# Kernel optimization log

Hardware: AMD Instinct MI355X
Metric: run time of the kernel (lower is better)

## Reference

```python
import jax, jax.numpy as jnp
import numpy as np

N = 131072        # total nodes (256 graphs x 512 nodes)
E = 2097152       # edges (avg degree 16)
F_IN = 64
HID = 64
T = 8             # timesteps
NUM_GRAPHS = 256
NPG = 512         # nodes per graph (uniform -> n >= T branch of _node_blur)
H_CLF = 64
CLASSES = 10
NUM_STEPS = 4
BETA = 0.9
THR = 1.0
SLOPE = 25.0      # snntorch surrogate.fast_sigmoid default slope

@jax.custom_vjp
def spike_fn(v):
    # heaviside forward, fast-sigmoid surrogate backward (snn.Leaky spike)
    return (v > 0).astype(v.dtype)

def _spk_fwd(v):
    return spike_fn(v), v

def _spk_bwd(v, g):
    return (g / (SLOPE * jnp.abs(v) + 1.0) ** 2,)

spike_fn.defvjp(_spk_fwd, _spk_bwd)

def gcn_conv(x, src, dst, w, b):
    # PyG GCNConv: add self loops, symmetric normalization, aggregate src->dst
    h = x @ w
    loop = jnp.arange(N, dtype=src.dtype)
    s = jnp.concatenate([src, loop])
    d = jnp.concatenate([dst, loop])
    deg = jax.ops.segment_sum(jnp.ones(s.shape, h.dtype), d, num_segments=N)
    dinv = jnp.where(deg > 0, jax.lax.rsqrt(jnp.maximum(deg, 1e-12)), 0.0)
    msg = h[s] * (dinv[s] * dinv[d])[:, None]          # [E+N, HID]
    return jax.ops.segment_sum(msg, d, num_segments=N) + b

def lif_rate(x):
    # snn.Leaky (reset_mechanism='subtract'): reset from previous mem (detached),
    # mem = beta*mem + x - reset*thr, spk = heaviside(mem - thr); mean spike rate.
    def step(mem, _):
        reset = jax.lax.stop_gradient((mem > THR).astype(x.dtype))
        mem = BETA * mem + x - reset * THR
        return mem, spike_fn(mem - THR)
    _, spks = jax.lax.scan(step, jnp.zeros_like(x), None, length=NUM_STEPS)
    return spks.mean(axis=0)

def node_blur(x):
    # uniform graphs, n = NPG >= T: reshape each graph to (r, T, F) and
    # combine chunks with weights linspace(thr, 0, r)
    r = NPG // T
    w = jnp.linspace(THR, 0.0, r, dtype=x.dtype)
    xg = x.reshape(NUM_GRAPHS, r, T, HID)
    return jnp.einsum('r,grtf->gtf', w, xg)             # [G, T, HID]

def setup_inputs() -> dict:
    key = jax.random.key(0)
    ks = jax.random.split(key, 8)
    x = jax.random.normal(ks[0], (N, F_IN), jnp.float32)
    edge_index = jax.random.randint(ks[1], (2, E), 0, N, jnp.int32)
    batch = (jnp.arange(N) // NPG).astype(jnp.int32)
    def lin(k, fi, fo):
        s = 1.0 / np.sqrt(fi)
        k1, k2 = jax.random.split(k)
        return (jax.random.uniform(k1, (fi, fo), jnp.float32, -s, s),
                jax.random.uniform(k2, (fo,), jnp.float32, -s, s))
    conv1_w, conv1_b = lin(ks[2], F_IN, HID)
    conv2_w, conv2_b = lin(ks[3], HID, HID)
    lin1_w, lin1_b = lin(ks[4], HID * T, H_CLF)
    lin2_w, lin2_b = lin(ks[5], H_CLF, H_CLF)
    lin3_w, lin3_b = lin(ks[6], H_CLF, CLASSES)
    return dict(x=x, edge_index=edge_index, batch=batch,
                conv1_w=conv1_w, conv1_b=conv1_b, conv2_w=conv2_w, conv2_b=conv2_b,
                lin1_w=lin1_w, lin1_b=lin1_b, lin2_w=lin2_w, lin2_b=lin2_b,
                lin3_w=lin3_w, lin3_b=lin3_b)

def reference(x, edge_index, batch, conv1_w, conv1_b, conv2_w, conv2_b,
              lin1_w, lin1_b, lin2_w, lin2_b, lin3_w, lin3_b):
    src, dst = edge_index[0], edge_index[1]
    h = gcn_conv(x, src, dst, conv1_w, conv1_b)
    h = jax.nn.relu(h)                                   # dropout: eval-mode identity
    h = gcn_conv(h, src, dst, conv2_w, conv2_b)
    z = node_blur(h)                                     # [G, T, HID]
    z = z.reshape(NUM_GRAPHS, T * HID)
    z = lif_rate(z @ lin1_w + lin1_b)
    z = lif_rate(z @ lin2_w + lin2_b)
    return z @ lin3_w + lin3_b                           # [G, CLASSES]
```

## Files before the change

kernel.cpp:

```cpp
#include <hip/hip_runtime.h>
#include <hip/hip_bf16.h>

#define NN 131072
#define EE 2097152
#define NG 256
#define TT 8
#define NB 512
#define NBLK 1024
#define SCAP 16
#define MAXW 32
#define OVFA_CAP 4096
#define OVFB_CAP 16384

__global__ __launch_bounds__(256) void k_zero_i(int* __restrict__ p, int n) {
  int i = blockIdx.x * 256 + threadIdx.x;
  if (i < n) p[i] = 0;
}

__global__ __launch_bounds__(256) void k_part2(const int* __restrict__ ei, int* __restrict__ pairs,
                                               int* __restrict__ cnt2, int* __restrict__ ovfAcnt,
                                               int2* __restrict__ ovfA) {
  __shared__ int lcur[NB];
  int tid = threadIdx.x, blk = blockIdx.x;
  lcur[tid] = 0; lcur[tid + 256] = 0;
  __syncthreads();
  int e0 = blk * (EE / NBLK);
#pragma unroll
  for (int i = 0; i < (EE / NBLK) / 256; ++i) {
    int e = e0 + i * 256 + tid;
    int s = ei[e], d = ei[EE + e];
    int b = d >> 8;
    int k = atomicAdd(&lcur[b], 1);
    if (k < SCAP)
      pairs[((size_t)blk * NB + b) * SCAP + k] = ((d & 255) << 17) | s;
    else {
      int oi = atomicAdd(ovfAcnt, 1);
      if (oi < OVFA_CAP) ovfA[oi] = make_int2(d, s);
    }
  }
  __syncthreads();
  cnt2[(size_t)blk * NB + tid] = min(lcur[tid], SCAP);
  cnt2[(size_t)blk * NB + tid + 256] = min(lcur[tid + 256], SCAP);
}

__global__ __launch_bounds__(256) void k_bucket(const int* __restrict__ pairs, const int* __restrict__ cnt2,
                                                int* __restrict__ col, int* __restrict__ cnt,
                                                const int* __restrict__ ovfAcnt, const int2* __restrict__ ovfA,
                                                int* __restrict__ ovfBcnt, int2* __restrict__ ovfB) {
  __shared__ int lcnt[256];
  __shared__ int lell[256 * MAXW];
  __shared__ int scnt[NBLK];
  int b = blockIdx.x, tid = threadIdx.x;
  lcnt[tid] = 0;
#pragma unroll
  for (int i = 0; i < NBLK / 256; ++i)
    scnt[tid + i * 256] = cnt2[(size_t)(tid + i * 256) * NB + b];
  __syncthreads();
  for (int idx = tid; idx < NBLK * SCAP; idx += 256) {
    int blk = idx >> 4, slot = idx & (SCAP - 1);
    if (slot < scnt[blk]) {
      int p = pairs[(size_t)blk * (NB * SCAP) + b * SCAP + slot];
      int s = p & 0x1FFFF, dl = p >> 17;
      int k = atomicAdd(&lcnt[dl], 1);
      if (k < MAXW) lell[dl * MAXW + k] = s;
      else {
        int oi = atomicAdd(ovfBcnt, 1);
        if (oi < OVFB_CAP) ovfB[oi] = make_int2(b * 256 + dl, s);
      }
    }
  }
  int na = min(*ovfAcnt, OVFA_CAP);
  for (int i = tid; i < na; i += 256) {
    int d = ovfA[i].x, s = ovfA[i].y;
    if ((d >> 8) == b) {
      int dl = d & 255;
      int k = atomicAdd(&lcnt[dl], 1);
      if (k < MAXW) lell[dl * MAXW + k] = s;
      else {
        int oi = atomicAdd(ovfBcnt, 1);
        if (oi < OVFB_CAP) ovfB[oi] = make_int2(d, s);
      }
    }
  }
  __syncthreads();
  int4* dst4 = (int4*)(col + (size_t)b * 256 * MAXW);
  const int4* src4 = (const int4*)lell;
#pragma unroll
  for (int i = 0; i < (256 * MAXW / 4) / 256; ++i)
    dst4[tid + i * 256] = src4[tid + i * 256];
  cnt[b * 256 + tid] = lcnt[tid];
}

__global__ __launch_bounds__(256) void k_gemm(const float* __restrict__ X, const float* __restrict__ W,
                                              const float* __restrict__ bias_in, int relu_bias,
                                              float* __restrict__ Y) {
  __shared__ float xs[64 * 64];
  __shared__ float ws[64 * 64];
  int tid = threadIdx.x;
  size_t row0 = (size_t)blockIdx.x * 64;
#pragma unroll
  for (int i = 0; i < 16; ++i) ws[tid + i * 256] = W[tid + i * 256];
#pragma unroll
  for (int i = 0; i < 4; ++i) {
    int idx = tid + i * 256;
    int r = idx >> 4, q = idx & 15;
    float4 v = ((const float4*)(X + (row0 + r) * 64))[q];
    if (relu_bias) {
      int c0 = q * 4;
      v.x = fmaxf(v.x + bias_in[c0 + 0], 0.f);
      v.y = fmaxf(v.y + bias_in[c0 + 1], 0.f);
      v.z = fmaxf(v.z + bias_in[c0 + 2], 0.f);
      v.w = fmaxf(v.w + bias_in[c0 + 3], 0.f);
    }
    *(float4*)&xs[idx * 4] = v;
  }
  __syncthreads();
  int c = tid & 63, rg = tid >> 6;
  float acc[16];
#pragma unroll
  for (int i = 0; i < 16; ++i) acc[i] = 0.f;
#pragma unroll 4
  for (int kq = 0; kq < 16; ++kq) {
    float w0 = ws[(kq * 4 + 0) * 64 + c];
    float w1 = ws[(kq * 4 + 1) * 64 + c];
    float w2 = ws[(kq * 4 + 2) * 64 + c];
    float w3 = ws[(kq * 4 + 3) * 64 + c];
#pragma unroll
    for (int i = 0; i < 16; ++i) {
      const float4 xv = *(const float4*)&xs[(rg + i * 4) * 64 + kq * 4];
      acc[i] += xv.x * w0 + xv.y * w1 + xv.z * w2 + xv.w * w3;
    }
  }
#pragma unroll
  for (int i = 0; i < 16; ++i)
    Y[(row0 + rg + (size_t)i * 4) * 64 + c] = acc[i];
}

__global__ __launch_bounds__(256) void k_gather_ell(const float* __restrict__ H, const int* __restrict__ cnt,
                                                    const int* __restrict__ col, float* __restrict__ agg) {
  int lane = threadIdx.x & 63;
  int n0 = (blockIdx.x * 4 + (threadIdx.x >> 6)) * 2;
  int n1 = n0 + 1;
  int deg0 = cnt[n0], deg1 = cnt[n1];
  float dn0 = rsqrtf((float)deg0 + 1.0f), dn1 = rsqrtf((float)deg1 + 1.0f);
  float acc0 = H[(size_t)n0 * 64 + lane] * (dn0 * dn0);
  float acc1 = H[(size_t)n1 * 64 + lane] * (dn1 * dn1);
  int m0 = min(deg0, MAXW), m1 = min(deg1, MAXW);
  const int* c0r = col + (size_t)n0 * MAXW;
  const int* c1r = col + (size_t)n1 * MAXW;
  int myc0 = (lane < m0) ? c0r[lane] : 0;
  int myc1 = (lane < m1) ? c1r[lane] : 0;
  float md0 = (lane < m0) ? rsqrtf((float)cnt[myc0] + 1.0f) : 0.f;
  float md1 = (lane < m1) ? rsqrtf((float)cnt[myc1] + 1.0f) : 0.f;
  int mm = max(m0, m1);
  for (int j = 0; j < mm; j += 4) {
    float h[8], cc[8];
#pragma unroll
    for (int k = 0; k < 4; ++k) {
      if (j + k < m0) {
        int s = __shfl(myc0, j + k);
        cc[k] = __shfl(md0, j + k);
        h[k] = H[(size_t)s * 64 + lane];
      } else { h[k] = 0.f; cc[k] = 0.f; }
      if (j + k < m1) {
        int s = __shfl(myc1, j + k);
        cc[4 + k] = __shfl(md1, j + k);
        h[4 + k] = H[(size_t)s * 64 + lane];
      } else { h[4 + k] = 0.f; cc[4 + k] = 0.f; }
    }
#pragma unroll
    for (int k = 0; k < 4; ++k) {
      acc0 += h[k] * (cc[k] * dn0);
      acc1 += h[4 + k] * (cc[4 + k] * dn1);
    }
  }
  agg[(size_t)n0 * 64 + lane] = acc0;
  agg[(size_t)n1 * 64 + lane] = acc1;
}

__global__ __launch_bounds__(64) void k_ovf(const int2* __restrict__ ovf, const int* __restrict__ ovfcnt,
                                            const int* __restrict__ cnt, const float* __restrict__ H,
                                            float* __restrict__ agg) {
  int lane = threadIdx.x;
  int n = min(*ovfcnt, OVFB_CAP);
  for (int i = blockIdx.x; i < n; i += gridDim.x) {
    int d = ovf[i].x, s = ovf[i].y;
    float v = H[(size_t)s * 64 + lane] * rsqrtf((float)cnt[s] + 1.0f) * rsqrtf((float)cnt[d] + 1.0f);
    atomicAdd(&agg[(size_t)d * 64 + lane], v);
  }
}

__global__ __launch_bounds__(256) void k_blur(const float* __restrict__ agg2, const float* __restrict__ b2,
                                              float* __restrict__ z) {
  int idx = blockIdx.x * 256 + threadIdx.x;
  if (idx >= NG * TT * 64) return;
  int f = idx & 63, t = (idx >> 6) & 7, g = idx >> 9;
  const float* base = agg2 + ((size_t)g * 512 + (size_t)t) * 64 + f;
  float acc = 0.f;
#pragma unroll
  for (int rr = 0; rr < 64; ++rr) {
    float w = (float)(63 - rr) * (1.0f / 63.0f);
    acc += w * base[(size_t)rr * 8 * 64];
  }
  z[idx] = acc + 32.0f * b2[f];
}

__global__ __launch_bounds__(64) void k_head(const float* __restrict__ z,
    const float* __restrict__ w1, const float* __restrict__ b1,
    const float* __restrict__ w2, const float* __restrict__ b2,
    const float* __restrict__ w3, const float* __restrict__ b3,
    float* __restrict__ out) {
  __shared__ float zs[512];
  __shared__ float r[64];
  int g = blockIdx.x, c = threadIdx.x;
#pragma unroll
  for (int i = 0; i < 8; ++i) zs[c + i * 64] = z[(size_t)g * 512 + c + i * 64];
  __syncthreads();
  float a = b1[c];
  for (int j = 0; j < 512; ++j) a += zs[j] * w1[j * 64 + c];
  float mem = 0.f, rate = 0.f;
#pragma unroll
  for (int s = 0; s < 4; ++s) {
    float reset = (mem > 1.0f) ? 1.0f : 0.0f;
    mem = 0.9f * mem + a - reset;
    if (mem - 1.0f > 0.0f) rate += 1.0f;
  }
  r[c] = rate * 0.25f;
  __syncthreads();
  float a2 = b2[c];
#pragma unroll
  for (int j = 0; j < 64; ++j) a2 += r[j] * w2[j * 64 + c];
  __syncthreads();
  mem = 0.f; rate = 0.f;
#pragma unroll
  for (int s = 0; s < 4; ++s) {
    float reset = (mem > 1.0f) ? 1.0f : 0.0f;
    mem = 0.9f * mem + a2 - reset;
    if (mem - 1.0f > 0.0f) rate += 1.0f;
  }
  r[c] = rate * 0.25f;
  __syncthreads();
  if (c < 10) {
    float o = b3[c];
#pragma unroll
    for (int j = 0; j < 64; ++j) o += r[j] * w3[j * 10 + c];
    out[(size_t)g * 10 + c] = o;
  }
}

extern "C" void kernel_launch(void* const* d_in, const int* in_sizes, int n_in,
                              void* d_out, int out_size, void* d_ws, size_t ws_size,
                              hipStream_t stream) {
  const float* x   = (const float*)d_in[0];
  const int*   ei  = (const int*)d_in[1];
  const float* c1w = (const float*)d_in[3];
  const float* c1b = (const float*)d_in[4];
  const float* c2w = (const float*)d_in[5];
  const float* c2b = (const float*)d_in[6];
  const float* l1w = (const float*)d_in[7];
  const float* l1b = (const float*)d_in[8];
  const float* l2w = (const float*)d_in[9];
  const float* l2b = (const float*)d_in[10];
  const float* l3w = (const float*)d_in[11];
  const float* l3b = (const float*)d_in[12];
  float* out = (float*)d_out;

  char* w = (char*)d_ws;
  size_t off = 0;
  float* bufA = (float*)(w + off); off += (size_t)NN * 64 * 4;
  float* bufB = (float*)(w + off); off += (size_t)NN * 64 * 4;
  int* col    = (int*)(w + off);   off += (size_t)NN * MAXW * 4;
  int* cnt    = (int*)(w + off);   off += (size_t)NN * 4;
  int* cnt2   = (int*)(w + off);   off += (size_t)NBLK * NB * 4;
  float* z    = (float*)(w + off); off += (size_t)NG * TT * 64 * 4;
  int* meta   = (int*)(w + off);   off += 16 * 4;
  int2* ovfA  = (int2*)(w + off);  off += (size_t)OVFA_CAP * 8;
  int2* ovfB  = (int2*)(w + off);  off += (size_t)OVFB_CAP * 8;
  int* ovfAcnt = meta;
  int* ovfBcnt = meta + 1;
  int* pairs   = (int*)bufA;

  k_zero_i<<<1, 256, 0, stream>>>(meta, 16);
  k_part2<<<NBLK, 256, 0, stream>>>(ei, pairs, cnt2, ovfAcnt, ovfA);
  k_bucket<<<NB, 256, 0, stream>>>(pairs, cnt2, col, cnt, ovfAcnt, ovfA, ovfBcnt, ovfB);

  k_gemm<<<NN / 64, 256, 0, stream>>>(x, c1w, nullptr, 0, bufA);
  k_gather_ell<<<NN / 8, 256, 0, stream>>>(bufA, cnt, col, bufB);
  k_ovf<<<32, 64, 0, stream>>>(ovfB, ovfBcnt, cnt, bufA, bufB);

  k_gemm<<<NN / 64, 256, 0, stream>>>(bufB, c2w, c1b, 1, bufA);
  k_gather_ell<<<NN / 8, 256, 0, stream>>>(bufA, cnt, col, bufB);
  k_ovf<<<32, 64, 0, stream>>>(ovfB, ovfBcnt, cnt, bufA, bufB);

  k_blur<<<NG * TT * 64 / 256, 256, 0, stream>>>(bufB, c2b, z);
  k_head<<<NG, 64, 0, stream>>>(z, l1w, l1b, l2w, l2b, l3w, l3b, out);
}
```

Measured before the change: 327.6 us.

## Move conv2 weight matmul past aggregation and blur, fuse overflow into gather

Because aggregation and the blur are linear, the conv2 weight multiply now runs after the node blur on the small per-graph tensor inside the head kernel, which removes the second full-size GEMM. Bias and ReLU are applied on the fly while the second gather loads each neighbour. The overflow edges are handled inside the gather kernel by a linear scan, replacing the separate atomic kernel. Per-block bucket counts are also stored as bytes instead of ints. The risk is that every warp scans the whole overflow list, which costs a lot if that list is large, and some floating-point results change slightly because of the reordering.

```diff
diff --git a/kernel.cpp b/kernel.cpp
--- a/kernel.cpp
+++ b/kernel.cpp
@@ -18,7 +18,7 @@
 }
 
 __global__ __launch_bounds__(256) void k_part2(const int* __restrict__ ei, int* __restrict__ pairs,
-                                               int* __restrict__ cnt2, int* __restrict__ ovfAcnt,
+                                               unsigned char* __restrict__ cnt2, int* __restrict__ ovfAcnt,
                                                int2* __restrict__ ovfA) {
   __shared__ int lcur[NB];
   int tid = threadIdx.x, blk = blockIdx.x;
@@ -39,17 +39,17 @@
     }
   }
   __syncthreads();
-  cnt2[(size_t)blk * NB + tid] = min(lcur[tid], SCAP);
-  cnt2[(size_t)blk * NB + tid + 256] = min(lcur[tid + 256], SCAP);
-}
-
-__global__ __launch_bounds__(256) void k_bucket(const int* __restrict__ pairs, const int* __restrict__ cnt2,
+  cnt2[(size_t)blk * NB + tid] = (unsigned char)min(lcur[tid], SCAP);
+  cnt2[(size_t)blk * NB + tid + 256] = (unsigned char)min(lcur[tid + 256], SCAP);
+}
+
+__global__ __launch_bounds__(256) void k_bucket(const int* __restrict__ pairs, const unsigned char* __restrict__ cnt2,
                                                 int* __restrict__ col, int* __restrict__ cnt,
                                                 const int* __restrict__ ovfAcnt, const int2* __restrict__ ovfA,
                                                 int* __restrict__ ovfBcnt, int2* __restrict__ ovfB) {
   __shared__ int lcnt[256];
   __shared__ int lell[256 * MAXW];
-  __shared__ int scnt[NBLK];
+  __shared__ unsigned char scnt[NBLK];
   int b = blockIdx.x, tid = threadIdx.x;
   lcnt[tid] = 0;
 #pragma unroll
@@ -58,7 +58,7 @@
   __syncthreads();
   for (int idx = tid; idx < NBLK * SCAP; idx += 256) {
     int blk = idx >> 4, slot = idx & (SCAP - 1);
-    if (slot < scnt[blk]) {
+    if (slot < (int)scnt[blk]) {
       int p = pairs[(size_t)blk * (NB * SCAP) + b * SCAP + slot];
       int s = p & 0x1FFFF, dl = p >> 17;
       int k = atomicAdd(&lcnt[dl], 1);
@@ -92,7 +92,6 @@
 }
 
 __global__ __launch_bounds__(256) void k_gemm(const float* __restrict__ X, const float* __restrict__ W,
-                                              const float* __restrict__ bias_in, int relu_bias,
                                               float* __restrict__ Y) {
   __shared__ float xs[64 * 64];
   __shared__ float ws[64 * 64];
@@ -105,13 +104,6 @@
     int idx = tid + i * 256;
     int r = idx >> 4, q = idx & 15;
     float4 v = ((const float4*)(X + (row0 + r) * 64))[q];
-    if (relu_bias) {
-      int c0 = q * 4;
-      v.x = fmaxf(v.x + bias_in[c0 + 0], 0.f);
-      v.y = fmaxf(v.y + bias_in[c0 + 1], 0.f);
-      v.z = fmaxf(v.z + bias_in[c0 + 2], 0.f);
-      v.w = fmaxf(v.w + bias_in[c0 + 3], 0.f);
-    }
     *(float4*)&xs[idx * 4] = v;
   }
   __syncthreads();
@@ -136,15 +128,23 @@
     Y[(row0 + rg + (size_t)i * 4) * 64 + c] = acc[i];
 }
 
-__global__ __launch_bounds__(256) void k_gather_ell(const float* __restrict__ H, const int* __restrict__ cnt,
-                                                    const int* __restrict__ col, float* __restrict__ agg) {
+template <int RELU>
+__global__ __launch_bounds__(256) void k_gather(const float* __restrict__ H, const int* __restrict__ cnt,
+                                                const int* __restrict__ col,
+                                                const int* __restrict__ ovfcnt, const int2* __restrict__ ovf,
+                                                const float* __restrict__ bias, float* __restrict__ agg) {
   int lane = threadIdx.x & 63;
   int n0 = (blockIdx.x * 4 + (threadIdx.x >> 6)) * 2;
   int n1 = n0 + 1;
+  float b = RELU ? bias[lane] : 0.f;
+  auto ld = [&](int s) -> float {
+    float v = H[(size_t)s * 64 + lane];
+    return RELU ? fmaxf(v + b, 0.f) : v;
+  };
   int deg0 = cnt[n0], deg1 = cnt[n1];
   float dn0 = rsqrtf((float)deg0 + 1.0f), dn1 = rsqrtf((float)deg1 + 1.0f);
-  float acc0 = H[(size_t)n0 * 64 + lane] * (dn0 * dn0);
-  float acc1 = H[(size_t)n1 * 64 + lane] * (dn1 * dn1);
+  float acc0 = ld(n0) * (dn0 * dn0);
+  float acc1 = ld(n1) * (dn1 * dn1);
   int m0 = min(deg0, MAXW), m1 = min(deg1, MAXW);
   const int* c0r = col + (size_t)n0 * MAXW;
   const int* c1r = col + (size_t)n1 * MAXW;
@@ -160,12 +160,12 @@
       if (j + k < m0) {
         int s = __shfl(myc0, j + k);
         cc[k] = __shfl(md0, j + k);
-        h[k] = H[(size_t)s * 64 + lane];
+        h[k] = ld(s);
       } else { h[k] = 0.f; cc[k] = 0.f; }
       if (j + k < m1) {
         int s = __shfl(myc1, j + k);
         cc[4 + k] = __shfl(md1, j + k);
-        h[4 + k] = H[(size_t)s * 64 + lane];
+        h[4 + k] = ld(s);
       } else { h[4 + k] = 0.f; cc[4 + k] = 0.f; }
     }
 #pragma unroll
@@ -174,50 +174,57 @@
       acc1 += h[4 + k] * (cc[4 + k] * dn1);
     }
   }
+  int na = min(*ovfcnt, OVFB_CAP);
+  for (int i = 0; i < na; ++i) {
+    int2 e = ovf[i];
+    if (e.x == n0) acc0 += ld(e.y) * (rsqrtf((float)cnt[e.y] + 1.0f) * dn0);
+    else if (e.x == n1) acc1 += ld(e.y) * (rsqrtf((float)cnt[e.y] + 1.0f) * dn1);
+  }
   agg[(size_t)n0 * 64 + lane] = acc0;
   agg[(size_t)n1 * 64 + lane] = acc1;
 }
 
-__global__ __launch_bounds__(64) void k_ovf(const int2* __restrict__ ovf, const int* __restrict__ ovfcnt,
-                                            const int* __restrict__ cnt, const float* __restrict__ H,
-                                            float* __restrict__ agg) {
-  int lane = threadIdx.x;
-  int n = min(*ovfcnt, OVFB_CAP);
-  for (int i = blockIdx.x; i < n; i += gridDim.x) {
-    int d = ovf[i].x, s = ovf[i].y;
-    float v = H[(size_t)s * 64 + lane] * rsqrtf((float)cnt[s] + 1.0f) * rsqrtf((float)cnt[d] + 1.0f);
-    atomicAdd(&agg[(size_t)d * 64 + lane], v);
-  }
-}
-
-__global__ __launch_bounds__(256) void k_blur(const float* __restrict__ agg2, const float* __restrict__ b2,
-                                              float* __restrict__ z) {
+__global__ __launch_bounds__(256) void k_blur(const float* __restrict__ G2, float* __restrict__ zpre) {
   int idx = blockIdx.x * 256 + threadIdx.x;
   if (idx >= NG * TT * 64) return;
   int f = idx & 63, t = (idx >> 6) & 7, g = idx >> 9;
-  const float* base = agg2 + ((size_t)g * 512 + (size_t)t) * 64 + f;
+  const float* base = G2 + ((size_t)g * 512 + (size_t)t) * 64 + f;
   float acc = 0.f;
 #pragma unroll
   for (int rr = 0; rr < 64; ++rr) {
     float w = (float)(63 - rr) * (1.0f / 63.0f);
     acc += w * base[(size_t)rr * 8 * 64];
   }
-  z[idx] = acc + 32.0f * b2[f];
-}
-
-__global__ __launch_bounds__(64) void k_head(const float* __restrict__ z,
-    const float* __restrict__ w1, const float* __restrict__ b1,
-    const float* __restrict__ w2, const float* __restrict__ b2,
-    const float* __restrict__ w3, const float* __restrict__ b3,
+  zpre[idx] = acc;
+}
+
+__global__ __launch_bounds__(64) void k_head(const float* __restrict__ zpre,
+    const float* __restrict__ cw, const float* __restrict__ cb,
+    const float* __restrict__ l1w, const float* __restrict__ l1b,
+    const float* __restrict__ l2w, const float* __restrict__ l2b,
+    const float* __restrict__ l3w, const float* __restrict__ l3b,
     float* __restrict__ out) {
+  __shared__ float zp[512];
   __shared__ float zs[512];
   __shared__ float r[64];
   int g = blockIdx.x, c = threadIdx.x;
 #pragma unroll
-  for (int i = 0; i < 8; ++i) zs[c + i * 64] = z[(size_t)g * 512 + c + i * 64];
-  __syncthreads();
-  float a = b1[c];
-  for (int j = 0; j < 512; ++j) a += zs[j] * w1[j * 64 + c];
+  for (int i = 0; i < 8; ++i) zp[c + i * 64] = zpre[(size_t)g * 512 + c + i * 64];
+  __syncthreads();
+  float zt[8];
+  float cbv = 32.0f * cb[c];
+#pragma unroll
+  for (int t = 0; t < 8; ++t) zt[t] = cbv;
+  for (int k = 0; k < 64; ++k) {
+    float w = cw[k * 64 + c];
+#pragma unroll
+    for (int t = 0; t < 8; ++t) zt[t] += zp[t * 64 + k] * w;
+  }
+#pragma unroll
+  for (int t = 0; t < 8; ++t) zs[t * 64 + c] = zt[t];
+  __syncthreads();
+  float a = l1b[c];
+  for (int j = 0; j < 512; ++j) a += zs[j] * l1w[j * 64 + c];
   float mem = 0.f, rate = 0.f;
 #pragma unroll
   for (int s = 0; s < 4; ++s) {
@@ -227,9 +234,9 @@
   }
   r[c] = rate * 0.25f;
   __syncthreads();
-  float a2 = b2[c];
-#pragma unroll
-  for (int j = 0; j < 64; ++j) a2 += r[j] * w2[j * 64 + c];
+  float a2 = l2b[c];
+#pragma unroll
+  for (int j = 0; j < 64; ++j) a2 += r[j] * l2w[j * 64 + c];
   __syncthreads();
   mem = 0.f; rate = 0.f;
 #pragma unroll
@@ -241,9 +248,9 @@
   r[c] = rate * 0.25f;
   __syncthreads();
   if (c < 10) {
-    float o = b3[c];
-#pragma unroll
-    for (int j = 0; j < 64; ++j) o += r[j] * w3[j * 10 + c];
+    float o = l3b[c];
+#pragma unroll
+    for (int j = 0; j < 64; ++j) o += r[j] * l3w[j * 10 + c];
     out[(size_t)g * 10 + c] = o;
   }
 }
@@ -271,8 +278,8 @@
   float* bufB = (float*)(w + off); off += (size_t)NN * 64 * 4;
   int* col    = (int*)(w + off);   off += (size_t)NN * MAXW * 4;
   int* cnt    = (int*)(w + off);   off += (size_t)NN * 4;
-  int* cnt2   = (int*)(w + off);   off += (size_t)NBLK * NB * 4;
-  float* z    = (float*)(w + off); off += (size_t)NG * TT * 64 * 4;
+  unsigned char* cnt2 = (unsigned char*)(w + off); off += (size_t)NBLK * NB;
+  float* zpre = (float*)(w + off); off += (size_t)NG * TT * 64 * 4;
   int* meta   = (int*)(w + off);   off += 16 * 4;
   int2* ovfA  = (int2*)(w + off);  off += (size_t)OVFA_CAP * 8;
   int2* ovfB  = (int2*)(w + off);  off += (size_t)OVFB_CAP * 8;
@@ -284,14 +291,11 @@
   k_part2<<<NBLK, 256, 0, stream>>>(ei, pairs, cnt2, ovfAcnt, ovfA);
   k_bucket<<<NB, 256, 0, stream>>>(pairs, cnt2, col, cnt, ovfAcnt, ovfA, ovfBcnt, ovfB);
 
-  k_gemm<<<NN / 64, 256, 0, stream>>>(x, c1w, nullptr, 0, bufA);
-  k_gather_ell<<<NN / 8, 256, 0, stream>>>(bufA, cnt, col, bufB);
-  k_ovf<<<32, 64, 0, stream>>>(ovfB, ovfBcnt, cnt, bufA, bufB);
-
-  k_gemm<<<NN / 64, 256, 0, stream>>>(bufB, c2w, c1b, 1, bufA);
-  k_gather_ell<<<NN / 8, 256, 0, stream>>>(bufA, cnt, col, bufB);
-  k_ovf<<<32, 64, 0, stream>>>(ovfB, ovfBcnt, cnt, bufA, bufB);
-
-  k_blur<<<NG * TT * 64 / 256, 256, 0, stream>>>(bufB, c2b, z);
-  k_head<<<NG, 64, 0, stream>>>(z, l1w, l1b, l2w, l2b, l3w, l3b, out);
-}
+  k_gemm<<<NN / 64, 256, 0, stream>>>(x, c1w, bufA);
+  k_gather<0><<<NN / 8, 256, 0, stream>>>(bufA, cnt, col, ovfBcnt, ovfB, nullptr, bufB);
+
+  k_gather<1><<<NN / 8, 256, 0, stream>>>(bufB, cnt, col, ovfBcnt, ovfB, c1b, bufA);
+
+  k_blur<<<NG * TT * 64 / 256, 256, 0, stream>>>(bufA, zpre);
+  k_head<<<NG, 64, 0, stream>>>(zpre, c2w, c2b, l1w, l1b, l2w, l2b, l3w, l3b, out);
+}
```

New measurement: 407.8 us. 24.5% more time.
